# Kernel tuning notes

Hardware: AMD Instinct MI355X
Metric: run time of the kernel (lower is better)

The kernel has to match this reference:

```python
import jax, jax.numpy as jnp
import numpy as np

B = 1024   # batch
N = 512    # points per sample (fixed by Linear(512,128))
G = 32     # voxel grid side (fixed: 5 stride-2 convs must reach 1^3)
CH = [1, 4, 16, 32, 64, 128]
BN_EPS = 1e-5


def _basis():
    # PointEmbed sinusoidal basis: hidden_dim=48 -> 8 freqs per axis, [3, 24]
    e = (2.0 ** np.arange(8)).astype(np.float32) * np.pi
    z = np.zeros(8, np.float32)
    b = np.stack([np.concatenate([e, z, z]),
                  np.concatenate([z, e, z]),
                  np.concatenate([z, z, e])])
    return jnp.asarray(b)


def setup_inputs() -> dict:
    key = jax.random.key(0)
    ks = jax.random.split(key, 16)
    inp = {
        "voxels": jax.random.normal(ks[0], (B, 1, G, G, G), jnp.float32),
        "centers": jax.random.uniform(ks[1], (B, N, 3), jnp.float32) * 2.0 - 1.0,
    }
    for i in range(5):
        cin, cout = CH[i], CH[i + 1]
        inp[f"W{i+1}"] = jax.random.normal(ks[2 + i], (cout, cin, 3, 3, 3), jnp.float32) * 0.05
        inp[f"b{i+1}"] = jnp.zeros((cout,), jnp.float32)
        inp[f"g{i+1}"] = jnp.ones((cout,), jnp.float32)
        inp[f"beta{i+1}"] = jnp.zeros((cout,), jnp.float32)
    inp["pe_w"] = jax.random.normal(ks[7], (51, 128), jnp.float32) * 0.05  # Linear(48+3, 128)
    inp["pe_b"] = jnp.zeros((128,), jnp.float32)
    inp["f1_w"] = jax.random.normal(ks[8], (128, 1), jnp.float32) * 0.05   # ff_128_1
    inp["f1_b"] = jnp.zeros((1,), jnp.float32)
    inp["f2_w"] = jax.random.normal(ks[9], (512, 128), jnp.float32) * 0.05  # ff_512_128
    inp["f2_b"] = jnp.zeros((128,), jnp.float32)
    return inp


def _conv_bn_relu(x, W, b, g, beta):
    # SparseConv3d(k=3, s=2, p=1) on fully-occupied grid == dense conv; BN in batch-stats mode
    y = jax.lax.conv_general_dilated(
        x, W, window_strides=(2, 2, 2), padding=[(1, 1)] * 3,
        dimension_numbers=("NCDHW", "OIDHW", "NCDHW"))
    y = y + b[None, :, None, None, None]
    m = jnp.mean(y, axis=(0, 2, 3, 4), keepdims=True)
    v = jnp.var(y, axis=(0, 2, 3, 4), keepdims=True)
    y = (y - m) * jax.lax.rsqrt(v + BN_EPS)
    y = y * g[None, :, None, None, None] + beta[None, :, None, None, None]
    return jax.nn.relu(y)


def reference(voxels, centers,
              W1, b1, g1, beta1, W2, b2, g2, beta2, W3, b3, g3, beta3,
              W4, b4, g4, beta4, W5, b5, g5, beta5,
              pe_w, pe_b, f1_w, f1_b, f2_w, f2_b):
    # --- PointEmbed branch ---
    basis = _basis()                                      # [3, 24]
    proj = jnp.einsum("bnd,de->bne", centers, basis)      # [B, N, 24]
    emb = jnp.concatenate([jnp.sin(proj), jnp.cos(proj), centers], axis=2)  # [B, N, 51]
    xc = emb @ pe_w + pe_b                                # [B, N, 128]
    xc = (xc @ f1_w + f1_b)[..., 0]                       # [B, N=512]
    xc = xc @ f2_w + f2_b                                 # [B, 128]
    # --- sparse conv stack (dense-occupancy equivalent) ---
    x = voxels
    for W, b, g, be in ((W1, b1, g1, beta1), (W2, b2, g2, beta2),
                        (W3, b3, g3, beta3), (W4, b4, g4, beta4),
                        (W5, b5, g5, beta5)):
        x = _conv_bn_relu(x, W, b, g, be)
    x = x.reshape(-1, 128)                                # [B,128,1,1,1] -> [B,128]
    return x + xc
```

## Files before the change

kernel.cpp:

```cpp
#include <hip/hip_runtime.h>
#include <hip/hip_bf16.h>

#ifndef M_PI
#define M_PI 3.14159265358979323846
#endif

#define BN_EPS 1e-5f

#define OFF_Y1   0ull
#define OFF_Y2   16777216ull
#define OFF_Y3   25165824ull
#define OFF_Y4   27262976ull
#define OFF_Y5   27787264ull
#define OFF_S    27918336ull
#define OFF_W2G  28442624ull
#define OFF_W3G  28444352ull
#define OFF_W5G  28458176ull
#define OFF_U    28523712ull
#define OFF_SP1  28523776ull
#define OFF_SP2  28524288ull
#define OFF_SP3  28526336ull
#define OFF_SP4  28530432ull
#define OFF_SP5  28538624ull
#define SP_TOTAL 31232
#define OFF_W4G  OFF_Y1

__device__ __forceinline__ float wred(float v) {
    for (int m = 32; m; m >>= 1) v += __shfl_xor(v, m, 64);
    return v;
}

__device__ __forceinline__ void async_copy16(const void* g, void* l) {
    __builtin_amdgcn_global_load_lds((const __attribute__((address_space(1))) void*)g,
                                     (__attribute__((address_space(3))) void*)l,
                                     16, 0, 0);
}

__device__ __forceinline__ unsigned short f2bf(float f) {
    unsigned int x = __float_as_uint(f);
    unsigned int r = (x + 0x7fffu + ((x >> 16) & 1u)) >> 16;
    return (unsigned short)r;
}
__device__ __forceinline__ float bf2f(unsigned short u) {
    return __uint_as_float(((unsigned int)u) << 16);
}

__global__ void k_prep_w(const float* __restrict__ W2, const float* __restrict__ W3,
                         const float* __restrict__ W5,
                         float* __restrict__ w2g, float* __restrict__ w3g,
                         float* __restrict__ w5g) {
    int idx = blockIdx.x * 256 + threadIdx.x;
    if (idx < 1728) {
        int co = idx & 15; int r = idx >> 4; int tap = r % 27; int ci = r / 27;
        w2g[idx] = W2[(co * 4 + ci) * 27 + tap];
        return;
    }
    idx -= 1728;
    if (idx < 13824) {
        int co = idx & 31; int r = idx >> 5; int tap = r % 27; int ci = r / 27;
        w3g[idx] = W3[(co * 16 + ci) * 27 + tap];
        return;
    }
    idx -= 13824;
    if (idx < 65536) {
        int co = idx & 127; int k = idx >> 7;
        int dx = k & 1, dy = (k >> 1) & 1, dz = (k >> 2) & 1, ci = k >> 3;
        w5g[idx] = W5[(co * 64 + ci) * 27 + (dz + 1) * 9 + (dy + 1) * 3 + (dx + 1)];
    }
}

__global__ void k_prep_w4(const float* __restrict__ W4, float* __restrict__ w4g) {
    int idx = blockIdx.x * 256 + threadIdx.x;
    if (idx < 55296) {
        int co = idx & 63; int r = idx >> 6;
        int tap = r % 27, ci = r / 27;
        w4g[idx] = W4[(co * 32 + ci) * 27 + tap];
    }
}

__global__ void k_prep_u(const float* __restrict__ pe_w, const float* __restrict__ pe_b,
                         const float* __restrict__ f1_w, const float* __restrict__ f1_b,
                         float* __restrict__ u) {
    int t = threadIdx.x;
    if (t < 51) {
        float acc = 0.f;
        for (int j = 0; j < 128; j++) acc += pe_w[t * 128 + j] * f1_w[j];
        u[t] = acc;
    } else if (t == 51) {
        float acc = f1_b[0];
        for (int j = 0; j < 128; j++) acc += pe_b[j] * f1_w[j];
        u[51] = acc;
    }
}

__global__ __launch_bounds__(256) void k_pe(const float* __restrict__ centers,
                                            const float* __restrict__ u,
                                            float* __restrict__ s) {
    __shared__ float us[52];
    int t = threadIdx.x;
    if (t < 52) us[t] = u[t];
    __syncthreads();
    int idx = blockIdx.x * 256 + t;
    float c3[3];
    c3[0] = centers[idx * 3 + 0];
    c3[1] = centers[idx * 3 + 1];
    c3[2] = centers[idx * 3 + 2];
    float acc = us[51] + c3[0] * us[48] + c3[1] * us[49] + c3[2] * us[50];
#pragma unroll
    for (int a = 0; a < 3; a++) {
#pragma unroll
        for (int f = 0; f < 8; f++) {
            float ang = c3[a] * (float)(M_PI * (double)(1 << f));
            float sv, cv;
            sincosf(ang, &sv, &cv);
            acc += sv * us[a * 8 + f] + cv * us[24 + a * 8 + f];
        }
    }
    s[idx] = acc;
}

__global__ __launch_bounds__(256) void k_c1(const float* __restrict__ vox,
                                            const float* __restrict__ W1,
                                            const float* __restrict__ b1,
                                            unsigned short* __restrict__ y1b,
                                            float* __restrict__ sp1) {
    __shared__ __align__(16) float slab[9 * 1024];
    __shared__ __align__(16) float wl[112];
    __shared__ float red2[32];
    int bid = blockIdx.x;
    int b = bid >> 1, q = bid & 1;
    int t = threadIdx.x;
    const float* vb = vox + (size_t)b * 32768;
    int wu = __builtin_amdgcn_readfirstlane(t >> 6);

    if (t < 108) { int tap = t >> 2, co = t & 3; wl[t] = W1[co * 27 + tap]; }
    if (q == 0) ((float4*)slab)[t] = make_float4(0.f, 0.f, 0.f, 0.f);

    int p0 = 16 * q;
    int s0 = q ? 7 : 0;
    {
        int s = s0;
        for (int i = 0; i < 5; i++) {
            int p = p0 - 1 + i;
            if (p >= 0) async_copy16(vb + p * 1024 + t * 4, slab + s * 1024 + wu * 256);
            s++; if (s == 9) s = 0;
        }
    }
    int yo = t >> 4, xo = t & 15;
    int e = 2 * xo;
    int eA = (e >= 2) ? e - 2 : 0;
    float mx0 = xo ? 1.f : 0.f;
    int iyc[3]; float myv[3];
#pragma unroll
    for (int ky = 0; ky < 3; ky++) {
        int iy = 2 * yo + ky - 1;
        myv[ky] = (iy < 0) ? 0.f : 1.f;
        iyc[ky] = (iy < 0) ? 0 : iy;
    }
    float bb0 = b1[0], bb1 = b1[1], bb2 = b1[2], bb3 = b1[3];
    float sums[4] = {0.f, 0.f, 0.f, 0.f}, sqs[4] = {0.f, 0.f, 0.f, 0.f};

    asm volatile("s_waitcnt vmcnt(0)" ::: "memory");
    __syncthreads();

    int s_win = s0;
    for (int j = 0; j < 4; j++) {
        int zq = 4 * q + j;
        if (j < 3) {
            int sp = s_win + 5; if (sp >= 9) sp -= 9;
            for (int i = 0; i < 4; i++) {
                int p = 4 * zq + 4 + i;
                async_copy16(vb + p * 1024 + t * 4, slab + sp * 1024 + wu * 256);
                sp++; if (sp == 9) sp = 0;
            }
        }
        int P[5];
        {
            int s = s_win;
#pragma unroll
            for (int i = 0; i < 5; i++) { P[i] = s * 1024; s++; if (s == 9) s = 0; }
        }
        float a0[4] = {bb0, bb1, bb2, bb3};
        float a1[4] = {bb0, bb1, bb2, bb3};
#pragma unroll
        for (int kz = 0; kz < 3; kz++) {
            const float* pz0 = slab + P[kz];
            const float* pz1 = slab + P[kz + 2];
#pragma unroll
            for (int ky = 0; ky < 3; ky++) {
                int ro = iyc[ky] * 32;
                float2 xa0 = *(const float2*)(pz0 + ro + eA);
                float2 xb0 = *(const float2*)(pz0 + ro + e);
                float2 xa1 = *(const float2*)(pz1 + ro + eA);
                float2 xb1 = *(const float2*)(pz1 + ro + e);
                float m1 = myv[ky], m0 = m1 * mx0;
                const float* wt = wl + (kz * 9 + ky * 3) * 4;
                float4 w0 = *(const float4*)(wt);
                float4 w1 = *(const float4*)(wt + 4);
                float4 w2 = *(const float4*)(wt + 8);
                float v00 = xa0.y * m0, v01 = xb0.x * m1, v02 = xb0.y * m1;
                float v10 = xa1.y * m0, v11 = xb1.x * m1, v12 = xb1.y * m1;
                a0[0] += v00 * w0.x + v01 * w1.x + v02 * w2.x;
                a0[1] += v00 * w0.y + v01 * w1.y + v02 * w2.y;
                a0[2] += v00 * w0.z + v01 * w1.z + v02 * w2.z;
                a0[3] += v00 * w0.w + v01 * w1.w + v02 * w2.w;
                a1[0] += v10 * w0.x + v11 * w1.x + v12 * w2.x;
                a1[1] += v10 * w0.y + v11 * w1.y + v12 * w2.y;
                a1[2] += v10 * w0.z + v11 * w1.z + v12 * w2.z;
                a1[3] += v10 * w0.w + v11 * w1.w + v12 * w2.w;
            }
        }
        size_t base = (size_t)b * 16384 + (size_t)(2 * zq) * 256 + t;
#pragma unroll
        for (int c = 0; c < 4; c++) {
            y1b[base + c * 4096] = f2bf(a0[c]);
            y1b[base + c * 4096 + 256] = f2bf(a1[c]);
            sums[c] += a0[c] + a1[c];
            sqs[c] += a0[c] * a0[c] + a1[c] * a1[c];
        }
        s_win += 4; if (s_win >= 9) s_win -= 9;
        asm volatile("s_waitcnt vmcnt(0)" ::: "memory");
        __syncthreads();
    }
    int lane = t & 63, w = t >> 6;
#pragma unroll
    for (int c = 0; c < 4; c++) { sums[c] = wred(sums[c]); sqs[c] = wred(sqs[c]); }
    if (lane == 0) {
#pragma unroll
        for (int c = 0; c < 4; c++) { red2[w * 8 + c] = sums[c]; red2[w * 8 + 4 + c] = sqs[c]; }
    }
    __syncthreads();
    if (t < 8) {
        int c = t >> 1, isq = t & 1;
        float acc = red2[isq * 4 + c] + red2[8 + isq * 4 + c] +
                    red2[16 + isq * 4 + c] + red2[24 + isq * 4 + c];
        atomicAdd(&sp1[(2 * c + isq) * 64 + (bid & 63)], acc);
    }
}

__global__ __launch_bounds__(256) void k_c2(const unsigned short* __restrict__ y1b,
                                            const float* __restrict__ w2g,
                                            const float* __restrict__ b2,
                                            const float* __restrict__ g1,
                                            const float* __restrict__ be1,
                                            const float* __restrict__ sp1,
                                            float* __restrict__ y2,
                                            float* __restrict__ sp2) {
    __shared__ __align__(16) unsigned short slab16[9216];
    __shared__ __align__(16) float wl[1728];
    __shared__ float adl[8];
    __shared__ float red[8];
    int t = threadIdx.x;
    int bid = blockIdx.x;
    int b = bid >> 1, q = bid & 1;
    int w = t >> 6, lane = t & 63;
    int wu = __builtin_amdgcn_readfirstlane(w);
    const unsigned short* yb = y1b + (size_t)b * 16384;
    if (q == 0) ((float2*)slab16)[t] = make_float2(0.f, 0.f);
    {
        int h = wu & 1;
        int ci0 = h * 2 + (lane >> 5);
        int g = lane & 31;
        int gs = g ^ (((g >> 3) & 3) << 1);
        const unsigned short* src0 = yb + ci0 * 4096 + gs * 8;
        int pstart = wu >> 1;
        if (q == 0 && pstart == 0) pstart = 2;
        for (int p = pstart; p < 9; p += 2) {
            int zi = 8 * q - 1 + p;
            async_copy16(src0 + zi * 256, slab16 + p * 1024 + h * 512);
        }
    }
    for (int i = t; i < 1728; i += 256) wl[i] = w2g[i];
    for (int row = w; row < 8; row += 4) {
        float v = wred(sp1[row * 64 + lane]);
        if (lane == 0) red[row] = v;
    }
    __syncthreads();
    if (t < 4) {
        float cnt = 4194304.0f;
        float m = red[2 * t] / cnt;
        float var = red[2 * t + 1] / cnt - m * m;
        float a = g1[t] * rsqrtf(var + BN_EPS);
        adl[t] = a; adl[4 + t] = be1[t] - m * a;
    }
    asm volatile("s_waitcnt vmcnt(0)" ::: "memory");
    __syncthreads();
    int zp = w >> 1;
    int cgo = __builtin_amdgcn_readfirstlane((w & 1) * 8);
    int yo = lane >> 3, xo = lane & 7;
    float my0 = yo ? 1.f : 0.f, mx0 = xo ? 1.f : 0.f;
    float mzw = (q == 0 && zp == 0) ? 0.f : 1.f;
    int yw3[3], sw3[3], xh3[3], xp3[3];
#pragma unroll
    for (int k = 0; k < 3; k++) {
        int yi = 2 * yo + k - 1; int yc = yi < 0 ? 0 : yi;
        yw3[k] = yc * 8;
        sw3[k] = ((yc >> 2) & 3) << 3;
        int xi = 2 * xo + k - 1; int xv = xi < 0 ? 0 : xi;
        xh3[k] = xv >> 1; xp3[k] = xv & 1;
    }
    float aa[4], dd[4];
#pragma unroll
    for (int c = 0; c < 4; c++) { aa[c] = adl[c]; dd[c] = adl[4 + c]; }
    float acc0[8], acc1[8];
#pragma unroll
    for (int c = 0; c < 8; c++) { acc0[c] = b2[cgo + c]; acc1[c] = acc0[c]; }
    for (int ci = 0; ci < 4; ci++) {
        float a = aa[ci], d = dd[ci];
        const unsigned short* pb16 = slab16 + zp * 4096 + ci * 256;
        const float* wci = wl + ci * 432 + cgo;
#pragma unroll
        for (int kz = 0; kz < 3; kz++) {
            const unsigned short* pl = pb16 + kz * 1024;
#pragma unroll
            for (int ky = 0; ky < 3; ky++) {
                int wb = yw3[ky], sw = sw3[ky];
#pragma unroll
                for (int kx = 0; kx < 3; kx++) {
                    int idx = (((wb + xh3[kx]) ^ sw) << 1) | xp3[kx];
                    float v0 = bf2f(pl[idx]);
                    float v1 = bf2f(pl[idx + 2048]);
                    float vb0 = fmaxf(a * v0 + d, 0.f);
                    float vb1 = fmaxf(a * v1 + d, 0.f);
                    if (kz == 0) vb0 *= mzw;
                    if (ky == 0) { vb0 *= my0; vb1 *= my0; }
                    if (kx == 0) { vb0 *= mx0; vb1 *= mx0; }
                    const float* wt = wci + (kz * 9 + ky * 3 + kx) * 16;
                    float4 wA = *(const float4*)(wt);
                    float4 wB = *(const float4*)(wt + 4);
                    acc0[0] += vb0 * wA.x; acc0[1] += vb0 * wA.y;
                    acc0[2] += vb0 * wA.z; acc0[3] += vb0 * wA.w;
                    acc0[4] += vb0 * wB.x; acc0[5] += vb0 * wB.y;
                    acc0[6] += vb0 * wB.z; acc0[7] += vb0 * wB.w;
                    acc1[0] += vb1 * wA.x; acc1[1] += vb1 * wA.y;
                    acc1[2] += vb1 * wA.z; acc1[3] += vb1 * wA.w;
                    acc1[4] += vb1 * wB.x; acc1[5] += vb1 * wB.y;
                    acc1[6] += vb1 * wB.z; acc1[7] += vb1 * wB.w;
                }
            }
        }
    }
    int z0 = 4 * q + 2 * zp;
    size_t ob = (size_t)b * 8192 + (size_t)cgo * 512 + z0 * 64 + lane;
#pragma unroll
    for (int c = 0; c < 8; c++) {
        y2[ob + c * 512] = acc0[c];
        y2[ob + c * 512 + 64] = acc1[c];
    }
    int slot = bid & 63;
#pragma unroll
    for (int c = 0; c < 8; c++) {
        float s_ = wred(acc0[c] + acc1[c]);
        float q_ = wred(acc0[c] * acc0[c] + acc1[c] * acc1[c]);
        if (lane == 0) {
            atomicAdd(&sp2[(2 * (cgo + c)) * 64 + slot], s_);
            atomicAdd(&sp2[(2 * (cgo + c) + 1) * 64 + slot], q_);
        }
    }
}

__global__ __launch_bounds__(256) void k_c3(const float* __restrict__ y2,
                                            const float* __restrict__ w3g,
                                            const float* __restrict__ b3,
                                            const float* __restrict__ g2,
                                            const float* __restrict__ be2,
                                            const float* __restrict__ sp2,
                                            float* __restrict__ y3,
                                            float* __restrict__ sp3) {
    __shared__ __align__(16) float in3[8192];
    __shared__ float adl[32], red[32];
    int t = threadIdx.x;
    int b = blockIdx.x;
    int w = t >> 6, lane = t & 63;
    int wu = __builtin_amdgcn_readfirstlane(w);
    const float* yb = y2 + (size_t)b * 8192;
    for (int j = 0; j < 8; j++) {
        int s = ((j << 2) + (lane >> 4)) & 7;
        async_copy16(yb + wu * 2048 + j * 256 + ((lane ^ s) << 2),
                     in3 + wu * 2048 + j * 256);
    }
    for (int row = w; row < 32; row += 4) {
        float v = wred(sp2[row * 64 + lane]);
        if (lane == 0) red[row] = v;
    }
    __syncthreads();
    if (t < 16) {
        float cnt = 524288.0f;
        float m = red[2 * t] / cnt;
        float var = red[2 * t + 1] / cnt - m * m;
        float a = g2[t] * rsqrtf(var + BN_EPS);
        adl[t] = a; adl[16 + t] = be2[t] - m * a;
    }
    asm volatile("s_waitcnt vmcnt(0)" ::: "memory");
    __syncthreads();
    int px = lane & 3, py = (lane >> 2) & 3, pz = lane >> 4;
    float mz0 = pz ? 1.f : 0.f, my0 = py ? 1.f : 0.f, mx0 = px ? 1.f : 0.f;
    int zb3[3], sz3[3], yv3[3], xv3[3];
#pragma unroll
    for (int k = 0; k < 3; k++) {
        int zi = 2 * pz + k - 1; int zc = zi < 0 ? 0 : zi;
        zb3[k] = zc * 64; sz3[k] = zc << 2;
        int yi = 2 * py + k - 1; int yc = yi < 0 ? 0 : yi;
        yv3[k] = yc * 8;
        int xi = 2 * px + k - 1; xv3[k] = xi < 0 ? 0 : xi;
    }
    int coh = wu & 1, cih = wu >> 1;
    int cgo = coh * 16;
    float acc[16];
#pragma unroll
    for (int c = 0; c < 16; c++) acc[c] = 0.f;
    for (int cii = 0; cii < 8; cii++) {
        int ci = cih * 8 + cii;
        float a = adl[ci], d = adl[16 + ci];
        const float* base = in3 + ci * 512;
        const float* wci = w3g + ci * 864 + cgo;
#pragma unroll
        for (int kz = 0; kz < 3; kz++) {
            int A1 = zb3[kz], sz = sz3[kz];
#pragma unroll
            for (int ky = 0; ky < 3; ky++) {
                int A2 = A1 + yv3[ky];
#pragma unroll
                for (int kx = 0; kx < 3; kx++) {
                    float v = base[(A2 + xv3[kx]) ^ sz];
                    float vb = fmaxf(a * v + d, 0.f);
                    if (kz == 0) vb *= mz0;
                    if (ky == 0) vb *= my0;
                    if (kx == 0) vb *= mx0;
                    const float* wr = wci + (kz * 9 + ky * 3 + kx) * 32;
#pragma unroll
                    for (int c = 0; c < 16; c++) acc[c] += vb * wr[c];
                }
            }
        }
    }
    __syncthreads();
    if (wu >= 2) {
        float* pp = in3 + (wu & 1) * 1280 + lane * 20;
#pragma unroll
        for (int c4 = 0; c4 < 4; c4++)
            *(float4*)(pp + c4 * 4) = make_float4(acc[c4*4], acc[c4*4+1], acc[c4*4+2], acc[c4*4+3]);
    }
    __syncthreads();
    if (wu < 2) {
        const float* pp = in3 + wu * 1280 + lane * 20;
#pragma unroll
        for (int c = 0; c < 16; c++) acc[c] += pp[c] + b3[cgo + c];
        size_t ob = (size_t)b * 2048 + lane;
#pragma unroll
        for (int c = 0; c < 16; c++) y3[ob + (size_t)(cgo + c) * 64] = acc[c];
        int slot = b & 63;
#pragma unroll
        for (int c = 0; c < 16; c++) {
            float s_ = wred(acc[c]), q_ = wred(acc[c] * acc[c]);
            if (lane == 0) {
                atomicAdd(&sp3[(2 * (cgo + c)) * 64 + slot], s_);
                atomicAdd(&sp3[(2 * (cgo + c) + 1) * 64 + slot], q_);
            }
        }
    }
}

__global__ __launch_bounds__(256) void k_c4(const float* __restrict__ y3,
                                            const float* __restrict__ w4g,
                                            const float* __restrict__ b4,
                                            const float* __restrict__ g3,
                                            const float* __restrict__ be3,
                                            const float* __restrict__ sp3,
                                            float* __restrict__ y4,
                                            float* __restrict__ sp4) {
    __shared__ __align__(16) float in4[16416];
    __shared__ float adb[64], red[64];
    int t = threadIdx.x;
    int bid = blockIdx.x;
    int bq = bid >> 2, coq = bid & 3;
    int w = t >> 6, lane = t & 63;
    int wu = __builtin_amdgcn_readfirstlane(w);
#pragma unroll
    for (int h = 0; h < 2; h++) {
        int bs2 = wu * 2 + h;
        const float* src = y3 + (size_t)(bq * 8 + bs2) * 2048 + lane * 4;
        for (int j = 0; j < 8; j++)
            async_copy16(src + j * 256, in4 + bs2 * 2052 + j * 256);
    }
    for (int row = w; row < 64; row += 4) {
        float v = wred(sp3[row * 64 + lane]);
        if (lane == 0) red[row] = v;
    }
    __syncthreads();
    if (t < 32) {
        float cnt = 65536.0f;
        float m = red[2 * t] / cnt;
        float var = red[2 * t + 1] / cnt - m * m;
        float a = g3[t] * rsqrtf(var + BN_EPS);
        adb[t] = a; adb[32 + t] = be3[t] - m * a;
    }
    asm volatile("s_waitcnt vmcnt(0)" ::: "memory");
    __syncthreads();
    int bs = lane >> 3, pos = lane & 7;
    int pz = pos >> 2, py = (pos >> 1) & 1, px = pos & 1;
    int z0 = 2 * pz - 1; if (z0 < 0) z0 = 0;
    int y0 = 2 * py - 1; if (y0 < 0) y0 = 0;
    int x0 = 2 * px - 1; if (x0 < 0) x0 = 0;
    int zo_[3] = {z0 * 16, 2 * pz * 16, (2 * pz + 1) * 16};
    int yo_[3] = {y0 * 4, 2 * py * 4, (2 * py + 1) * 4};
    int xo_[3] = {x0, 2 * px, 2 * px + 1};
    float mz = pz ? 1.f : 0.f, my = py ? 1.f : 0.f, mx = px ? 1.f : 0.f;
    float acc[16];
#pragma unroll
    for (int c = 0; c < 16; c++) acc[c] = 0.f;
    const float* inb = in4 + bs * 2052;
    for (int cii = 0; cii < 8; cii++) {
        int ci = wu * 8 + cii;
        float a = adb[ci], d = adb[32 + ci];
        const float* inc = inb + ci * 64;
        const float* wcb = w4g + ci * 1728 + coq * 16;
#pragma unroll
        for (int kz = 0; kz < 3; kz++)
#pragma unroll
            for (int ky = 0; ky < 3; ky++)
#pragma unroll
                for (int kx = 0; kx < 3; kx++) {
                    float v = inc[zo_[kz] + yo_[ky] + xo_[kx]];
                    float vb = fmaxf(a * v + d, 0.f);
                    if (kz == 0) vb *= mz;
                    if (ky == 0) vb *= my;
                    if (kx == 0) vb *= mx;
                    const float* wr = wcb + (kz * 9 + ky * 3 + kx) * 64;
#pragma unroll
                    for (int c = 0; c < 16; c++) acc[c] += vb * wr[c];
                }
    }
    __syncthreads();
    if (wu > 0) {
        float* pp = in4 + (wu - 1) * 1280 + lane * 20;
#pragma unroll
        for (int c4 = 0; c4 < 4; c4++)
            *(float4*)(pp + c4 * 4) = make_float4(acc[c4*4], acc[c4*4+1], acc[c4*4+2], acc[c4*4+3]);
    }
    __syncthreads();
    if (wu == 0) {
#pragma unroll
        for (int p = 0; p < 3; p++) {
            const float* pp = in4 + p * 1280 + lane * 20;
#pragma unroll
            for (int c = 0; c < 16; c++) acc[c] += pp[c];
        }
        int bfull = bq * 8 + bs;
        size_t ob = (size_t)bfull * 512 + pos;
        int slot = bid & 63;
#pragma unroll
        for (int c = 0; c < 16; c++) {
            float vv = acc[c] + b4[coq * 16 + c];
            y4[ob + (size_t)(coq * 16 + c) * 8] = vv;
            acc[c] = vv;
        }
#pragma unroll
        for (int c = 0; c < 16; c++) {
            float s_ = wred(acc[c]), q_ = wred(acc[c] * acc[c]);
            if (lane == 0) {
                atomicAdd(&sp4[(2 * (coq * 16 + c)) * 64 + slot], s_);
                atomicAdd(&sp4[(2 * (coq * 16 + c) + 1) * 64 + slot], q_);
            }
        }
    }
}

__global__ __launch_bounds__(512) void k_c5(const float* __restrict__ y4,
                                            const float* __restrict__ w5g,
                                            const float* __restrict__ b5,
                                            const float* __restrict__ g4,
                                            const float* __restrict__ be4,
                                            const float* __restrict__ sp4,
                                            float* __restrict__ y5,
                                            float* __restrict__ sp5) {
    __shared__ __align__(16) float A[2048];
    __shared__ float P[512];
    __shared__ float ad[128], red[128];
    int t = threadIdx.x;
    int bq = blockIdx.x;
    int w = t >> 6, lane = t & 63;
    for (int row = w; row < 128; row += 8) {
        float v = wred(sp4[row * 64 + lane]);
        if (lane == 0) red[row] = v;
    }
    __syncthreads();
    if (t < 64) {
        float cnt = 8192.0f;
        float m = red[2 * t] / cnt;
        float var = red[2 * t + 1] / cnt - m * m;
        float a = g4[t] * rsqrtf(var + BN_EPS);
        ad[t] = a; ad[64 + t] = be4[t] - m * a;
    }
    __syncthreads();
    {
        int bs = t >> 7, k0 = (t & 127) << 2;
        float4 vv = *(const float4*)(y4 + (size_t)(bq * 4 + bs) * 512 + k0);
        int ci = k0 >> 3;
        float a = ad[ci], d = ad[64 + ci];
        float4 o;
        o.x = fmaxf(a * vv.x + d, 0.f);
        o.y = fmaxf(a * vv.y + d, 0.f);
        o.z = fmaxf(a * vv.z + d, 0.f);
        o.w = fmaxf(a * vv.w + d, 0.f);
        *(float4*)(A + bs * 512 + k0) = o;
    }
    __syncthreads();
    int bs = w & 3, kh = w >> 2;
    float acc0 = 0.f, acc1 = 0.f;
    const float* Ab = A + bs * 512 + kh * 256;
    const float* wp = w5g + kh * 32768 + lane * 2;
#pragma unroll 8
    for (int k = 0; k < 256; k++) {
        float2 wv = *(const float2*)(wp + k * 128);
        float av = Ab[k];
        acc0 += av * wv.x;
        acc1 += av * wv.y;
    }
    if (kh == 0) {
        P[bs * 128 + lane * 2] = acc0;
        P[bs * 128 + lane * 2 + 1] = acc1;
    }
    __syncthreads();
    if (kh == 1) {
        float f0 = acc0 + P[bs * 128 + lane * 2] + b5[lane * 2];
        float f1 = acc1 + P[bs * 128 + lane * 2 + 1] + b5[lane * 2 + 1];
        *(float2*)(y5 + (size_t)(bq * 4 + bs) * 128 + lane * 2) = make_float2(f0, f1);
        P[bs * 128 + lane * 2] = f0;
        P[bs * 128 + lane * 2 + 1] = f1;
    }
    __syncthreads();
    if (t < 128) {
        float s = 0.f, q = 0.f;
        for (int bb = 0; bb < 4; bb++) {
            float vv = P[bb * 128 + t];
            s += vv; q += vv * vv;
        }
        int slot = bq & 63;
        atomicAdd(&sp5[(2 * t) * 64 + slot], s);
        atomicAdd(&sp5[(2 * t + 1) * 64 + slot], q);
    }
}

__global__ __launch_bounds__(512) void k_f2(const float* __restrict__ s,
                                            const float* __restrict__ f2w,
                                            const float* __restrict__ f2b,
                                            const float* __restrict__ g5,
                                            const float* __restrict__ be5,
                                            const float* __restrict__ sp5,
                                            const float* __restrict__ y5,
                                            float* __restrict__ out) {
    __shared__ __align__(16) float A[2048];
    __shared__ float P[512];
    __shared__ float ad[256], red[256];
    int t = threadIdx.x;
    int bq = blockIdx.x;
    int w = t >> 6, lane = t & 63;
    for (int row = w; row < 256; row += 8) {
        float v = wred(sp5[row * 64 + lane]);
        if (lane == 0) red[row] = v;
    }
    __syncthreads();
    if (t < 128) {
        float cnt = 1024.0f;
        float m = red[2 * t] / cnt;
        float var = red[2 * t + 1] / cnt - m * m;
        float a = g5[t] * rsqrtf(var + BN_EPS);
        ad[t] = a; ad[128 + t] = be5[t] - m * a;
    }
    {
        int bs = t >> 7, k0 = (t & 127) << 2;
        float4 vv = *(const float4*)(s + (size_t)(bq * 4 + bs) * 512 + k0);
        *(float4*)(A + bs * 512 + k0) = vv;
    }
    __syncthreads();
    int bs = w & 3, kh = w >> 2;
    float acc0 = 0.f, acc1 = 0.f;
    const float* Ab = A + bs * 512 + kh * 256;
    const float* wp = f2w + kh * 32768 + lane * 2;
#pragma unroll 8
    for (int k = 0; k < 256; k++) {
        float2 wv = *(const float2*)(wp + k * 128);
        float av = Ab[k];
        acc0 += av * wv.x;
        acc1 += av * wv.y;
    }
    if (kh == 0) {
        P[bs * 128 + lane * 2] = acc0;
        P[bs * 128 + lane * 2 + 1] = acc1;
    }
    __syncthreads();
    if (kh == 1) {
        int b = bq * 4 + bs;
        int co = lane * 2;
        float2 vy = *(const float2*)(y5 + (size_t)b * 128 + co);
        float f0 = acc0 + P[bs * 128 + co] + f2b[co] +
                   fmaxf(ad[co] * vy.x + ad[128 + co], 0.f);
        float f1 = acc1 + P[bs * 128 + co + 1] + f2b[co + 1] +
                   fmaxf(ad[co + 1] * vy.y + ad[128 + co + 1], 0.f);
        *(float2*)(out + (size_t)b * 128 + co) = make_float2(f0, f1);
    }
}

extern "C" void kernel_launch(void* const* d_in, const int* in_sizes, int n_in,
                              void* d_out, int out_size, void* d_ws, size_t ws_size,
                              hipStream_t stream) {
    const float* vox     = (const float*)d_in[0];
    const float* centers = (const float*)d_in[1];
    const float* W1   = (const float*)d_in[2];
    const float* b1   = (const float*)d_in[3];
    const float* g1   = (const float*)d_in[4];
    const float* be1  = (const float*)d_in[5];
    const float* W2   = (const float*)d_in[6];
    const float* b2   = (const float*)d_in[7];
    const float* g2   = (const float*)d_in[8];
    const float* be2  = (const float*)d_in[9];
    const float* W3   = (const float*)d_in[10];
    const float* b3   = (const float*)d_in[11];
    const float* g3   = (const float*)d_in[12];
    const float* be3  = (const float*)d_in[13];
    const float* W4   = (const float*)d_in[14];
    const float* b4   = (const float*)d_in[15];
    const float* g4   = (const float*)d_in[16];
    const float* be4  = (const float*)d_in[17];
    const float* W5   = (const float*)d_in[18];
    const float* b5   = (const float*)d_in[19];
    const float* g5   = (const float*)d_in[20];
    const float* be5  = (const float*)d_in[21];
    const float* pe_w = (const float*)d_in[22];
    const float* pe_b = (const float*)d_in[23];
    const float* f1_w = (const float*)d_in[24];
    const float* f1_b = (const float*)d_in[25];
    const float* f2_w = (const float*)d_in[26];
    const float* f2_b = (const float*)d_in[27];

    float* ws  = (float*)d_ws;
    unsigned short* y1b = (unsigned short*)(ws + OFF_Y1);
    float* y2  = ws + OFF_Y2;
    float* y3  = ws + OFF_Y3;
    float* y4  = ws + OFF_Y4;
    float* y5  = ws + OFF_Y5;
    float* s   = ws + OFF_S;
    float* w2g = ws + OFF_W2G;
    float* w3g = ws + OFF_W3G;
    float* w4g = ws + OFF_W4G;
    float* w5g = ws + OFF_W5G;
    float* u   = ws + OFF_U;
    float* sp1 = ws + OFF_SP1;
    float* sp2 = ws + OFF_SP2;
    float* sp3 = ws + OFF_SP3;
    float* sp4 = ws + OFF_SP4;
    float* sp5 = ws + OFF_SP5;

    hipMemsetAsync((void*)sp1, 0, SP_TOTAL * sizeof(float), stream);
    k_prep_w<<<317, 256, 0, stream>>>(W2, W3, W5, w2g, w3g, w5g);
    k_prep_u<<<1, 64, 0, stream>>>(pe_w, pe_b, f1_w, f1_b, u);
    k_pe<<<2048, 256, 0, stream>>>(centers, u, s);
    k_c1<<<2048, 256, 0, stream>>>(vox, W1, b1, y1b, sp1);
    k_c2<<<2048, 256, 0, stream>>>(y1b, w2g, b2, g1, be1, sp1, y2, sp2);
    k_prep_w4<<<216, 256, 0, stream>>>(W4, w4g);
    k_c3<<<1024, 256, 0, stream>>>(y2, w3g, b3, g2, be2, sp2, y3, sp3);
    k_c4<<<512, 256, 0, stream>>>(y3, w4g, b4, g3, be3, sp3, y4, sp4);
    k_c5<<<256, 512, 0, stream>>>(y4, w5g, b5, g4, be4, sp4, y5, sp5);
    k_f2<<<256, 512, 0, stream>>>(s, f2_w, f2_b, g5, be5, sp5, y5, (float*)d_out);
}
```

Measured before the change: 269.3 us.

## Restructure conv2 to one block per sample with z-column register reuse

Conv2 now processes a whole sample per block, and each wave computes 4 output channels across all 8 output z-slices. Each loaded input value is reused across the three kz taps by sliding along a 17-entry register column, which removes the duplicated halo loads and the redundant BN/ReLU evaluation of the old z-split. The memset of the stats partials is folded into the weight prep kernel to save a launch. The costs are more registers (a 32-entry accumulator array plus the column), larger LDS use, and half as many blocks.

```diff
diff --git a/kernel.cpp b/kernel.cpp
--- a/kernel.cpp
+++ b/kernel.cpp
@@ -48,7 +48,7 @@
 __global__ void k_prep_w(const float* __restrict__ W2, const float* __restrict__ W3,
                          const float* __restrict__ W5,
                          float* __restrict__ w2g, float* __restrict__ w3g,
-                         float* __restrict__ w5g) {
+                         float* __restrict__ w5g, float* __restrict__ sp) {
     int idx = blockIdx.x * 256 + threadIdx.x;
     if (idx < 1728) {
         int co = idx & 15; int r = idx >> 4; int tap = r % 27; int ci = r / 27;
@@ -66,7 +66,10 @@
         int co = idx & 127; int k = idx >> 7;
         int dx = k & 1, dy = (k >> 1) & 1, dz = (k >> 2) & 1, ci = k >> 3;
         w5g[idx] = W5[(co * 64 + ci) * 27 + (dz + 1) * 9 + (dy + 1) * 3 + (dx + 1)];
-    }
+        return;
+    }
+    idx -= 65536;
+    if (idx < SP_TOTAL) sp[idx] = 0.f;
 }
 
 __global__ void k_prep_w4(const float* __restrict__ W4, float* __restrict__ w4g) {
@@ -246,28 +249,25 @@
                                             const float* __restrict__ sp1,
                                             float* __restrict__ y2,
                                             float* __restrict__ sp2) {
-    __shared__ __align__(16) unsigned short slab16[9216];
+    __shared__ __align__(16) unsigned short slab16[17408];
     __shared__ __align__(16) float wl[1728];
     __shared__ float adl[8];
     __shared__ float red[8];
     int t = threadIdx.x;
-    int bid = blockIdx.x;
-    int b = bid >> 1, q = bid & 1;
+    int b = blockIdx.x;
     int w = t >> 6, lane = t & 63;
     int wu = __builtin_amdgcn_readfirstlane(w);
     const unsigned short* yb = y1b + (size_t)b * 16384;
-    if (q == 0) ((float2*)slab16)[t] = make_float2(0.f, 0.f);
+    if (t < 128) ((float4*)slab16)[t] = make_float4(0.f, 0.f, 0.f, 0.f);
     {
         int h = wu & 1;
         int ci0 = h * 2 + (lane >> 5);
         int g = lane & 31;
         int gs = g ^ (((g >> 3) & 3) << 1);
         const unsigned short* src0 = yb + ci0 * 4096 + gs * 8;
-        int pstart = wu >> 1;
-        if (q == 0 && pstart == 0) pstart = 2;
-        for (int p = pstart; p < 9; p += 2) {
-            int zi = 8 * q - 1 + p;
-            async_copy16(src0 + zi * 256, slab16 + p * 1024 + h * 512);
+        for (int s = 1 + (wu >> 1); s <= 16; s += 2) {
+            int zi = s - 1;
+            async_copy16(src0 + zi * 256, slab16 + s * 1024 + h * 512);
         }
     }
     for (int i = t; i < 1728; i += 256) wl[i] = w2g[i];
@@ -285,76 +285,77 @@
     }
     asm volatile("s_waitcnt vmcnt(0)" ::: "memory");
     __syncthreads();
-    int zp = w >> 1;
-    int cgo = __builtin_amdgcn_readfirstlane((w & 1) * 8);
+    int cgo = __builtin_amdgcn_readfirstlane(wu * 4);
     int yo = lane >> 3, xo = lane & 7;
-    float my0 = yo ? 1.f : 0.f, mx0 = xo ? 1.f : 0.f;
-    float mzw = (q == 0 && zp == 0) ? 0.f : 1.f;
-    int yw3[3], sw3[3], xh3[3], xp3[3];
+    int yw3[3], sw3[3]; float mY[3];
+    int xh3[3], xp3[3]; float mX[3];
 #pragma unroll
     for (int k = 0; k < 3; k++) {
         int yi = 2 * yo + k - 1; int yc = yi < 0 ? 0 : yi;
-        yw3[k] = yc * 8;
-        sw3[k] = ((yc >> 2) & 3) << 3;
+        yw3[k] = yc * 8; sw3[k] = ((yc >> 2) & 3) << 3;
+        mY[k] = yi < 0 ? 0.f : 1.f;
         int xi = 2 * xo + k - 1; int xv = xi < 0 ? 0 : xi;
         xh3[k] = xv >> 1; xp3[k] = xv & 1;
+        mX[k] = xi < 0 ? 0.f : 1.f;
     }
     float aa[4], dd[4];
 #pragma unroll
     for (int c = 0; c < 4; c++) { aa[c] = adl[c]; dd[c] = adl[4 + c]; }
-    float acc0[8], acc1[8];
-#pragma unroll
-    for (int c = 0; c < 8; c++) { acc0[c] = b2[cgo + c]; acc1[c] = acc0[c]; }
+    float bq[4];
+#pragma unroll
+    for (int j = 0; j < 4; j++) bq[j] = b2[cgo + j];
+    float acc[8][4];
+#pragma unroll
+    for (int z = 0; z < 8; z++)
+#pragma unroll
+        for (int j = 0; j < 4; j++) acc[z][j] = bq[j];
     for (int ci = 0; ci < 4; ci++) {
         float a = aa[ci], d = dd[ci];
-        const unsigned short* pb16 = slab16 + zp * 4096 + ci * 256;
+        const unsigned short* base = slab16 + ci * 256;
         const float* wci = wl + ci * 432 + cgo;
 #pragma unroll
-        for (int kz = 0; kz < 3; kz++) {
-            const unsigned short* pl = pb16 + kz * 1024;
-#pragma unroll
-            for (int ky = 0; ky < 3; ky++) {
-                int wb = yw3[ky], sw = sw3[ky];
-#pragma unroll
-                for (int kx = 0; kx < 3; kx++) {
-                    int idx = (((wb + xh3[kx]) ^ sw) << 1) | xp3[kx];
-                    float v0 = bf2f(pl[idx]);
-                    float v1 = bf2f(pl[idx + 2048]);
-                    float vb0 = fmaxf(a * v0 + d, 0.f);
-                    float vb1 = fmaxf(a * v1 + d, 0.f);
-                    if (kz == 0) vb0 *= mzw;
-                    if (ky == 0) { vb0 *= my0; vb1 *= my0; }
-                    if (kx == 0) { vb0 *= mx0; vb1 *= mx0; }
-                    const float* wt = wci + (kz * 9 + ky * 3 + kx) * 16;
-                    float4 wA = *(const float4*)(wt);
-                    float4 wB = *(const float4*)(wt + 4);
-                    acc0[0] += vb0 * wA.x; acc0[1] += vb0 * wA.y;
-                    acc0[2] += vb0 * wA.z; acc0[3] += vb0 * wA.w;
-                    acc0[4] += vb0 * wB.x; acc0[5] += vb0 * wB.y;
-                    acc0[6] += vb0 * wB.z; acc0[7] += vb0 * wB.w;
-                    acc1[0] += vb1 * wA.x; acc1[1] += vb1 * wA.y;
-                    acc1[2] += vb1 * wA.z; acc1[3] += vb1 * wA.w;
-                    acc1[4] += vb1 * wB.x; acc1[5] += vb1 * wB.y;
-                    acc1[6] += vb1 * wB.z; acc1[7] += vb1 * wB.w;
+        for (int ky = 0; ky < 3; ky++) {
+#pragma unroll
+            for (int kx = 0; kx < 3; kx++) {
+                float m = mY[ky] * mX[kx];
+                int idx = (((yw3[ky] + xh3[kx]) ^ sw3[ky]) << 1) | xp3[kx];
+                float4 wz0 = *(const float4*)(wci + (ky * 3 + kx) * 16);
+                float4 wz1 = *(const float4*)(wci + (9 + ky * 3 + kx) * 16);
+                float4 wz2 = *(const float4*)(wci + (18 + ky * 3 + kx) * 16);
+                float r[17];
+                r[0] = 0.f;
+#pragma unroll
+                for (int s = 1; s <= 16; s++) {
+                    float v = bf2f(base[s * 1024 + idx]);
+                    r[s] = fmaxf(a * v + d, 0.f) * m;
+                }
+#pragma unroll
+                for (int z = 0; z < 8; z++) {
+                    float rA = r[2 * z], rB = r[2 * z + 1], rC = r[2 * z + 2];
+                    acc[z][0] += rA * wz0.x + rB * wz1.x + rC * wz2.x;
+                    acc[z][1] += rA * wz0.y + rB * wz1.y + rC * wz2.y;
+                    acc[z][2] += rA * wz0.z + rB * wz1.z + rC * wz2.z;
+                    acc[z][3] += rA * wz0.w + rB * wz1.w + rC * wz2.w;
                 }
             }
         }
     }
-    int z0 = 4 * q + 2 * zp;
-    size_t ob = (size_t)b * 8192 + (size_t)cgo * 512 + z0 * 64 + lane;
-#pragma unroll
-    for (int c = 0; c < 8; c++) {
-        y2[ob + c * 512] = acc0[c];
-        y2[ob + c * 512 + 64] = acc1[c];
-    }
-    int slot = bid & 63;
-#pragma unroll
-    for (int c = 0; c < 8; c++) {
-        float s_ = wred(acc0[c] + acc1[c]);
-        float q_ = wred(acc0[c] * acc0[c] + acc1[c] * acc1[c]);
+    size_t ob = (size_t)b * 8192 + (size_t)cgo * 512 + lane;
+#pragma unroll
+    for (int j = 0; j < 4; j++)
+#pragma unroll
+        for (int z = 0; z < 8; z++)
+            y2[ob + j * 512 + z * 64] = acc[z][j];
+    int slot = b & 63;
+#pragma unroll
+    for (int j = 0; j < 4; j++) {
+        float s_ = 0.f, q_ = 0.f;
+#pragma unroll
+        for (int z = 0; z < 8; z++) { s_ += acc[z][j]; q_ += acc[z][j] * acc[z][j]; }
+        s_ = wred(s_); q_ = wred(q_);
         if (lane == 0) {
-            atomicAdd(&sp2[(2 * (cgo + c)) * 64 + slot], s_);
-            atomicAdd(&sp2[(2 * (cgo + c) + 1) * 64 + slot], q_);
+            atomicAdd(&sp2[(2 * (cgo + j)) * 64 + slot], s_);
+            atomicAdd(&sp2[(2 * (cgo + j) + 1) * 64 + slot], q_);
         }
     }
 }
@@ -752,12 +753,11 @@
     float* sp4 = ws + OFF_SP4;
     float* sp5 = ws + OFF_SP5;
 
-    hipMemsetAsync((void*)sp1, 0, SP_TOTAL * sizeof(float), stream);
-    k_prep_w<<<317, 256, 0, stream>>>(W2, W3, W5, w2g, w3g, w5g);
+    k_prep_w<<<439, 256, 0, stream>>>(W2, W3, W5, w2g, w3g, w5g, sp1);
     k_prep_u<<<1, 64, 0, stream>>>(pe_w, pe_b, f1_w, f1_b, u);
     k_pe<<<2048, 256, 0, stream>>>(centers, u, s);
     k_c1<<<2048, 256, 0, stream>>>(vox, W1, b1, y1b, sp1);
-    k_c2<<<2048, 256, 0, stream>>>(y1b, w2g, b2, g1, be1, sp1, y2, sp2);
+    k_c2<<<1024, 256, 0, stream>>>(y1b, w2g, b2, g1, be1, sp1, y2, sp2);
     k_prep_w4<<<216, 256, 0, stream>>>(W4, w4g);
     k_c3<<<1024, 256, 0, stream>>>(y2, w3g, b3, g2, be2, sp2, y3, sp3);
     k_c4<<<512, 256, 0, stream>>>(y3, w4g, b4, g3, be3, sp3, y4, sp4);
```

New measurement: 317.4 us. 17.9% more time.
